# Optimization experiments

Measured on AMD Instinct MI355X. Metric: run time of the kernel, lower is better.

The kernel has to match this reference:

```python
import jax, jax.numpy as jnp
import numpy as np

T = 8           # timesteps
VTH = 1.0       # IFNode v_threshold (spikingjelly default)
ALPHA = 2.0     # ATan surrogate alpha (spikingjelly default)
BN_EPS = 1e-5

@jax.custom_vjp
def atan_spike(x):
    # Heaviside(x) with ATan surrogate gradient
    return (x >= 0.0).astype(x.dtype)

def _spike_fwd(x):
    return atan_spike(x), x

def _spike_bwd(x, g):
    sg = (ALPHA / 2.0) / (1.0 + (jnp.pi / 2.0 * ALPHA * x) ** 2)
    return (g * sg,)

atan_spike.defvjp(_spike_fwd, _spike_bwd)

def maxpool2x2(x):  # [B,C,H,W] -> [B,C,H/2,W/2]
    return jax.lax.reduce_window(x, -jnp.inf, jax.lax.max,
                                 (1, 1, 2, 2), (1, 1, 2, 2), 'VALID')

def setup_inputs() -> dict:
    key = jax.random.key(0)
    k0, k1, k2 = jax.random.split(key, 3)
    B, C = 128, 128
    x = jax.random.uniform(k0, (B, 1, 28, 28), jnp.float32)
    conv_w = jax.random.normal(k1, (C, 1, 3, 3), jnp.float32) * 0.3
    bn_gamma = jnp.ones((C,), jnp.float32)
    bn_beta = jnp.zeros((C,), jnp.float32)
    bn_mean = jnp.zeros((C,), jnp.float32)
    bn_var = jnp.ones((C,), jnp.float32)
    fc_w = jax.random.normal(k2, (10, C * 14 * 14), jnp.float32) * 0.01
    return dict(x=x, conv_w=conv_w, bn_gamma=bn_gamma, bn_beta=bn_beta,
                bn_mean=bn_mean, bn_var=bn_var, fc_w=fc_w)

def reference(x, conv_w, bn_gamma, bn_beta, bn_mean, bn_var, fc_w):
    B = x.shape[0]
    # stateless conv + BN(eval): identical for all T repeated timesteps, compute once
    y = jax.lax.conv_general_dilated(
        x, conv_w, window_strides=(1, 1), padding=((1, 1), (1, 1)),
        dimension_numbers=('NCHW', 'OIHW', 'NCHW'))
    scale = (bn_gamma * jax.lax.rsqrt(bn_var + BN_EPS))[None, :, None, None]
    pre = (y - bn_mean[None, :, None, None]) * scale + bn_beta[None, :, None, None]

    def step(carry, _):
        v1, v2 = carry
        # IFNode 1: integrate, fire, hard reset to 0
        v1 = v1 + pre
        s1 = atan_spike(v1 - VTH)
        v1 = v1 * (1.0 - s1)
        f = maxpool2x2(s1).reshape(B, -1)        # [B, C*14*14]
        # IFNode 2 after linear
        v2 = v2 + f @ fc_w.T                      # [B, 10]
        s2 = atan_spike(v2 - VTH)
        v2 = v2 * (1.0 - s2)
        return (v1, v2), s2

    v1_0 = jnp.zeros_like(pre)
    v2_0 = jnp.zeros((B, 10), pre.dtype)
    _, spikes = jax.lax.scan(step, (v1_0, v2_0), None, length=T)  # [T,B,10]
    return spikes.mean(0)  # firing rate [B,10]
```

## Files before the change

kernel.cpp:

```cpp
#include <hip/hip_runtime.h>

#define T 8
#define VTH 1.0f
#define BN_EPS 1e-5f
#define CG 16
#define NG (128 / CG)

__global__ __launch_bounds__(256) void k_conv_if_pool(
    const float* __restrict__ x,
    const float* __restrict__ conv_w,
    const float* __restrict__ gamma,
    const float* __restrict__ beta,
    const float* __restrict__ mean,
    const float* __restrict__ var,
    unsigned char* __restrict__ f)
{
    __shared__ float xs[30 * 30];
    const int blk = blockIdx.x;
    const int b = blk / NG;
    const int g = blk - b * NG;
    const int tid = threadIdx.x;

    for (int i = tid; i < 900; i += 256) xs[i] = 0.0f;
    __syncthreads();
    const float* xb = x + b * 784;
    for (int i = tid; i < 784; i += 256) {
        int h = i / 28, w = i - h * 28;
        xs[(h + 1) * 30 + (w + 1)] = xb[i];
    }
    __syncthreads();

    if (tid >= 196) return;
    const int ph = tid / 14, pw = tid - ph * 14;

    float patch[16];
    const int base = (2 * ph) * 30 + 2 * pw;
    #pragma unroll
    for (int r = 0; r < 4; r++)
        #pragma unroll
        for (int cc = 0; cc < 4; cc++)
            patch[r * 4 + cc] = xs[base + r * 30 + cc];

    for (int ci = 0; ci < CG; ci++) {
        const int c = g * CG + ci;
        const float* wc = conv_w + c * 9;
        float wv[9];
        #pragma unroll
        for (int i = 0; i < 9; i++) wv[i] = wc[i];
        const float sc = gamma[c] * rsqrtf(var[c] + BN_EPS);
        const float sh = beta[c] - mean[c] * sc;

        unsigned int bits = 0;
        #pragma unroll
        for (int dy = 0; dy < 2; dy++) {
            #pragma unroll
            for (int dx = 0; dx < 2; dx++) {
                float y = 0.0f;
                #pragma unroll
                for (int kh = 0; kh < 3; kh++)
                    #pragma unroll
                    for (int kw = 0; kw < 3; kw++)
                        y += patch[(dy + kh) * 4 + (dx + kw)] * wv[kh * 3 + kw];
                const float p = y * sc + sh;
                float v = 0.0f;
                #pragma unroll
                for (int t = 0; t < T; t++) {
                    v += p;
                    if (v - VTH >= 0.0f) { bits |= (1u << t); v = 0.0f; }
                }
            }
        }
        f[(b * 128 + c) * 196 + tid] = (unsigned char)bits;
    }
}

__global__ __launch_bounds__(256) void k_fc_if(
    const unsigned char* __restrict__ f,
    const float* __restrict__ fc_w,
    float* __restrict__ out)
{
    const int blk = blockIdx.x;
    const int b = blk / 10;
    const int o = blk - b * 10;
    const int tid = threadIdx.x;
    const int lane = tid & 63;
    const int wave = tid >> 6;

    const unsigned int* fm = (const unsigned int*)(f + b * 25088);
    const float4* fw = (const float4*)(fc_w + o * 25088);

    float acc[T];
    #pragma unroll
    for (int t = 0; t < T; t++) acc[t] = 0.0f;

    for (int i = tid; i < 25088 / 4; i += 256) {
        const unsigned int m4 = fm[i];
        const float4 w = fw[i];
        const float wj[4] = {w.x, w.y, w.z, w.w};
        #pragma unroll
        for (int j = 0; j < 4; j++) {
            const unsigned int m = (m4 >> (8 * j)) & 0xffu;
            #pragma unroll
            for (int t = 0; t < T; t++) {
                if (m & (1u << t)) acc[t] += wj[j];
            }
        }
    }

    __shared__ float red[4][T];
    #pragma unroll
    for (int t = 0; t < T; t++) {
        float v = acc[t];
        #pragma unroll
        for (int off = 32; off > 0; off >>= 1)
            v += __shfl_down(v, off, 64);
        if (lane == 0) red[wave][t] = v;
    }
    __syncthreads();

    if (tid == 0) {
        float v2 = 0.0f, cnt = 0.0f;
        #pragma unroll
        for (int t = 0; t < T; t++) {
            const float a = red[0][t] + red[1][t] + red[2][t] + red[3][t];
            v2 += a;
            if (v2 - VTH >= 0.0f) { cnt += 1.0f; v2 = 0.0f; }
        }
        out[b * 10 + o] = cnt * (1.0f / (float)T);
    }
}

extern "C" void kernel_launch(void* const* d_in, const int* in_sizes, int n_in,
                              void* d_out, int out_size, void* d_ws, size_t ws_size,
                              hipStream_t stream) {
    const float* x      = (const float*)d_in[0];
    const float* conv_w = (const float*)d_in[1];
    const float* gamma  = (const float*)d_in[2];
    const float* beta   = (const float*)d_in[3];
    const float* mean   = (const float*)d_in[4];
    const float* var    = (const float*)d_in[5];
    const float* fc_w   = (const float*)d_in[6];
    float* out = (float*)d_out;

    unsigned char* f = (unsigned char*)d_ws;

    k_conv_if_pool<<<128 * NG, 256, 0, stream>>>(x, conv_w, gamma, beta, mean, var, f);
    k_fc_if<<<128 * 10, 256, 0, stream>>>(f, fc_w, out);
}
```

Baseline: 119.9 us.

## Compute five FC outputs per block to reuse spike loads, branchless FMA accumulate

The FC kernel now has each 512-thread block handle one batch row and five output neurons. Each spike word is loaded once and applied to five weight rows instead of being re-read once per output. The conditional adds become bit-times-weight FMAs, which removes divergent branches but does more arithmetic and uses 40 accumulators per thread. The conv kernel halves its channels per block to get more blocks and fully unrolls the channel loop. The FC grid shrinks to 256 blocks, which could leave compute units underused.

```diff
diff --git a/kernel.cpp b/kernel.cpp
--- a/kernel.cpp
+++ b/kernel.cpp
@@ -3,7 +3,7 @@
 #define T 8
 #define VTH 1.0f
 #define BN_EPS 1e-5f
-#define CG 16
+#define CG 8
 #define NG (128 / CG)
 
 __global__ __launch_bounds__(256) void k_conv_if_pool(
@@ -41,6 +41,7 @@
         for (int cc = 0; cc < 4; cc++)
             patch[r * 4 + cc] = xs[base + r * 30 + cc];
 
+    #pragma unroll
     for (int ci = 0; ci < CG; ci++) {
         const int c = g * CG + ci;
         const float* wc = conv_w + c * 9;
@@ -74,59 +75,79 @@
     }
 }
 
-__global__ __launch_bounds__(256) void k_fc_if(
+__global__ __launch_bounds__(512) void k_fc_if(
     const unsigned char* __restrict__ f,
     const float* __restrict__ fc_w,
     float* __restrict__ out)
 {
     const int blk = blockIdx.x;
-    const int b = blk / 10;
-    const int o = blk - b * 10;
+    const int b = blk >> 1;
+    const int og = blk & 1;
     const int tid = threadIdx.x;
     const int lane = tid & 63;
     const int wave = tid >> 6;
 
     const unsigned int* fm = (const unsigned int*)(f + b * 25088);
-    const float4* fw = (const float4*)(fc_w + o * 25088);
+    const float4* fw0 = (const float4*)(fc_w + (og * 5 + 0) * 25088);
+    const float4* fw1 = (const float4*)(fc_w + (og * 5 + 1) * 25088);
+    const float4* fw2 = (const float4*)(fc_w + (og * 5 + 2) * 25088);
+    const float4* fw3 = (const float4*)(fc_w + (og * 5 + 3) * 25088);
+    const float4* fw4 = (const float4*)(fc_w + (og * 5 + 4) * 25088);
 
-    float acc[T];
+    float acc[T][5];
     #pragma unroll
-    for (int t = 0; t < T; t++) acc[t] = 0.0f;
+    for (int t = 0; t < T; t++)
+        #pragma unroll
+        for (int o = 0; o < 5; o++) acc[t][o] = 0.0f;
 
-    for (int i = tid; i < 25088 / 4; i += 256) {
+    for (int i = tid; i < 25088 / 4; i += 512) {
         const unsigned int m4 = fm[i];
-        const float4 w = fw[i];
-        const float wj[4] = {w.x, w.y, w.z, w.w};
+        float4 w[5] = {fw0[i], fw1[i], fw2[i], fw3[i], fw4[i]};
         #pragma unroll
         for (int j = 0; j < 4; j++) {
-            const unsigned int m = (m4 >> (8 * j)) & 0xffu;
+            const float wj[5] = {((const float*)&w[0])[j], ((const float*)&w[1])[j],
+                                 ((const float*)&w[2])[j], ((const float*)&w[3])[j],
+                                 ((const float*)&w[4])[j]};
             #pragma unroll
             for (int t = 0; t < T; t++) {
-                if (m & (1u << t)) acc[t] += wj[j];
+                const float bit = (float)((m4 >> (8 * j + t)) & 1u);
+                #pragma unroll
+                for (int o = 0; o < 5; o++)
+                    acc[t][o] = fmaf(bit, wj[o], acc[t][o]);
             }
         }
     }
 
-    __shared__ float red[4][T];
+    __shared__ float red[8][T * 5];
     #pragma unroll
-    for (int t = 0; t < T; t++) {
-        float v = acc[t];
+    for (int t = 0; t < T; t++)
         #pragma unroll
-        for (int off = 32; off > 0; off >>= 1)
-            v += __shfl_down(v, off, 64);
-        if (lane == 0) red[wave][t] = v;
+        for (int o = 0; o < 5; o++) {
+            float v = acc[t][o];
+            #pragma unroll
+            for (int off = 32; off > 0; off >>= 1)
+                v += __shfl_down(v, off, 64);
+            if (lane == 0) red[wave][t * 5 + o] = v;
+        }
+    __syncthreads();
+
+    __shared__ float tot[T * 5];
+    if (tid < T * 5) {
+        float s = 0.0f;
+        #pragma unroll
+        for (int wv = 0; wv < 8; wv++) s += red[wv][tid];
+        tot[tid] = s;
     }
     __syncthreads();
 
-    if (tid == 0) {
+    if (tid < 5) {
         float v2 = 0.0f, cnt = 0.0f;
         #pragma unroll
         for (int t = 0; t < T; t++) {
-            const float a = red[0][t] + red[1][t] + red[2][t] + red[3][t];
-            v2 += a;
+            v2 += tot[t * 5 + tid];
             if (v2 - VTH >= 0.0f) { cnt += 1.0f; v2 = 0.0f; }
         }
-        out[b * 10 + o] = cnt * (1.0f / (float)T);
+        out[b * 10 + og * 5 + tid] = cnt * (1.0f / (float)T);
     }
 }
 
@@ -145,5 +166,5 @@
     unsigned char* f = (unsigned char*)d_ws;
 
     k_conv_if_pool<<<128 * NG, 256, 0, stream>>>(x, conv_w, gamma, beta, mean, var, f);
-    k_fc_if<<<128 * 10, 256, 0, stream>>>(f, fc_w, out);
+    k_fc_if<<<128 * 2, 512, 0, stream>>>(f, fc_w, out);
 }
```

New measurement: 116.7 us. 1.03x faster.
